# Kernel tuning notes

Measured on AMD Instinct MI355X. Metric: run time of the kernel, lower is better.

The kernel has to match this reference:

```python
import jax, jax.numpy as jnp
import numpy as np

N_NODES = 500_000
N_EDGES = 16_000_000


def gcn_conv(x, src, dst, ew, W, b, n_nodes):
    # PyG GCNConv: add self-loops (weight 1), symmetric normalization,
    # message = norm * (x @ W)[src], aggregate sum at dst, then + bias.
    loop = jnp.arange(n_nodes, dtype=src.dtype)
    src_f = jnp.concatenate([src, loop])
    dst_f = jnp.concatenate([dst, loop])
    ew_f = jnp.concatenate([ew, jnp.ones((n_nodes,), dtype=ew.dtype)])
    deg = jax.ops.segment_sum(ew_f, dst_f, num_segments=n_nodes)  # in-degree incl. self-loop
    dis = jnp.where(deg > 0, jax.lax.rsqrt(jnp.maximum(deg, 1e-12)), 0.0)
    norm = dis[src_f] * ew_f * dis[dst_f]  # [E+N]
    h = x @ W  # [N, out]
    msg = h[src_f] * norm[:, None]  # gather + scale
    out = jax.ops.segment_sum(msg, dst_f, num_segments=n_nodes)  # scatter-add
    return out + b


def setup_inputs() -> dict:
    key = jax.random.key(0)
    k = jax.random.split(key, 8)
    x = jax.random.normal(k[0], (N_NODES, 1), dtype=jnp.float32)
    edge_index = jax.random.randint(k[1], (2, N_EDGES), 0, N_NODES, dtype=jnp.int64)
    edge_weight = jax.random.uniform(k[2], (N_EDGES,), dtype=jnp.float32)
    W1 = jax.random.normal(k[3], (1, 16), dtype=jnp.float32)
    b1 = jax.random.normal(k[4], (16,), dtype=jnp.float32) * 0.1
    W2 = jax.random.normal(k[5], (16, 2), dtype=jnp.float32)
    b2 = jax.random.normal(k[6], (2,), dtype=jnp.float32) * 0.1
    return {"x": x, "edge_index": edge_index, "edge_weight": edge_weight,
            "W1": W1, "b1": b1, "W2": W2, "b2": b2}


def reference(x, edge_index, edge_weight, W1, b1, W2, b2):
    src, dst = edge_index[0], edge_index[1]
    n = x.shape[0]
    h = gcn_conv(x, src, dst, edge_weight, W1, b1, n)
    h = jax.nn.relu(h)
    # F.dropout(training=self.training): eval mode -> identity
    h = gcn_conv(h, src, dst, edge_weight, W2, b2, n)
    s = jnp.sum(h, axis=0)[None, :]  # [1, 2]
    return jax.nn.softmax(s, axis=1)
```

## Files before the change

### kernel.cpp

```cpp
#include <hip/hip_runtime.h>
#include <math.h>

constexpr int N_NODES   = 500000;
constexpr int N_EDGES   = 16000000;
constexpr int BSHIFT    = 12;
constexpr int BSZ       = 1 << BSHIFT;
constexpr int NB        = (N_NODES + BSZ - 1) / BSZ;
constexpr int CHK       = 6144;
constexpr int NCHK      = (N_EDGES + CHK - 1) / CHK;
constexpr int SPB_SHIFT = 4;
constexpr int SPB       = 1 << SPB_SHIFT;


__global__ __launch_bounds__(256) void k_count1(const int* __restrict__ dst,
                                                unsigned* __restrict__ counts) {
    __shared__ unsigned hist[NB];
    int c = blockIdx.x;
    for (int t = threadIdx.x; t < NB; t += 256) hist[t] = 0;
    __syncthreads();
    int lo = c * CHK, hi = min(lo + CHK, N_EDGES);
    for (int e = lo + threadIdx.x; e < hi; e += 256)
        atomicAdd(&hist[dst[e] >> BSHIFT], 1u);
    __syncthreads();
    for (int b = threadIdx.x; b < NB; b += 256)
        counts[(size_t)b * NCHK + c] = hist[b];
}

__global__ __launch_bounds__(256) void k_rowscan(const unsigned* __restrict__ counts,
                                                 unsigned* __restrict__ bases,
                                                 unsigned* __restrict__ rowsum) {
    __shared__ unsigned tile[256];
    __shared__ unsigned carry;
    int b = blockIdx.x;
    if (threadIdx.x == 0) carry = 0;
    __syncthreads();
    for (int t0 = 0; t0 < NCHK; t0 += 256) {
        int c = t0 + threadIdx.x;
        unsigned v = (c < NCHK) ? counts[(size_t)b * NCHK + c] : 0u;
        tile[threadIdx.x] = v;
        __syncthreads();
#pragma unroll
        for (int off = 1; off < 256; off <<= 1) {
            unsigned u = (threadIdx.x >= off) ? tile[threadIdx.x - off] : 0u;
            __syncthreads();
            tile[threadIdx.x] += u;
            __syncthreads();
        }
        unsigned excl = tile[threadIdx.x] - v;
        if (c < NCHK) bases[(size_t)b * NCHK + c] = carry + excl;
        __syncthreads();
        if (threadIdx.x == 0) carry += tile[255];
        __syncthreads();
    }
    if (threadIdx.x == 0) rowsum[b] = carry;
}

__global__ __launch_bounds__(128) void k_bucketscan(const unsigned* __restrict__ rowsum,
                                                    unsigned* __restrict__ offsets1) {
    __shared__ unsigned tile[128];
    int t = threadIdx.x;
    unsigned v = (t < NB) ? rowsum[t] : 0u;
    tile[t] = v;
    __syncthreads();
#pragma unroll
    for (int off = 1; off < 128; off <<= 1) {
        unsigned u = (t >= off) ? tile[t - off] : 0u;
        __syncthreads();
        tile[t] += u;
        __syncthreads();
    }
    if (t < NB) offsets1[t] = tile[t] - v;
    if (t == 0) offsets1[NB] = tile[127];
}

__global__ __launch_bounds__(256) void k_scatter1(const int* __restrict__ src,
                                                  const int* __restrict__ dst,
                                                  const float* __restrict__ w,
                                                  const unsigned* __restrict__ bases,
                                                  const unsigned* __restrict__ offsets1,
                                                  uint2* __restrict__ A) {
    __shared__ uint2    buf[CHK];
    __shared__ unsigned hist[NB];
    __shared__ unsigned coff[NB + 1];
    __shared__ unsigned cur[NB];
    __shared__ int      gbase[NB];
    int c = blockIdx.x;
    int lo = c * CHK, hi = min(lo + CHK, N_EDGES);
    int n = hi - lo;
    for (int t = threadIdx.x; t < NB; t += 256) { hist[t] = 0; cur[t] = 0; }
    __syncthreads();
    for (int e = lo + threadIdx.x; e < hi; e += 256)
        atomicAdd(&hist[dst[e] >> BSHIFT], 1u);
    __syncthreads();
    {
        __shared__ unsigned sc[128];
        int t = threadIdx.x;
        if (t < 128) sc[t] = (t < NB) ? hist[t] : 0u;
        __syncthreads();
#pragma unroll
        for (int off = 1; off < 128; off <<= 1) {
            unsigned u = 0;
            if (t < 128 && t >= off) u = sc[t - off];
            __syncthreads();
            if (t < 128) sc[t] += u;
            __syncthreads();
        }
        if (t < NB) coff[t] = sc[t] - hist[t];
        if (t == 0) coff[NB] = (unsigned)n;
        __syncthreads();
        if (t < NB)
            gbase[t] = (int)(offsets1[t] + bases[(size_t)t * NCHK + c]) - (int)coff[t];
    }
    __syncthreads();
    for (int e = lo + threadIdx.x; e < hi; e += 256) {
        int d = dst[e];
        int b = d >> BSHIFT;
        unsigned p = coff[b] + atomicAdd(&cur[b], 1u);
        buf[p] = make_uint2(((unsigned)(d & (BSZ - 1)) << 19) | (unsigned)src[e],
                            __float_as_uint(w[e]));
    }
    __syncthreads();
    for (int i = threadIdx.x; i < n; i += 256) {
        int blo = 0, bhi = NB;
        while (blo + 1 < bhi) {
            int m = (blo + bhi) >> 1;
            if ((int)coff[m] <= i) blo = m; else bhi = m;
        }
        A[gbase[blo] + i] = buf[i];
    }
}

__device__ __forceinline__ void slice_bounds(const unsigned* offsets1,
                                             int& b, int& e0, int& e1) {
    b = blockIdx.x >> SPB_SHIFT;
    int s = blockIdx.x & (SPB - 1);
    int base = (int)offsets1[b];
    int len  = (int)offsets1[b + 1] - base;
    e0 = base + (int)(((long long)len * s) >> SPB_SHIFT);
    e1 = base + (int)(((long long)len * (s + 1)) >> SPB_SHIFT);
}

__global__ __launch_bounds__(256) void k_deg(const uint2* __restrict__ A,
                                             const unsigned* __restrict__ offsets1,
                                             float* __restrict__ staging) {
    __shared__ float bins[BSZ];
    for (int i = threadIdx.x; i < BSZ; i += 256) bins[i] = 0.0f;
    int b, e0, e1;
    slice_bounds(offsets1, b, e0, e1);
    __syncthreads();
    for (int e = e0 + threadIdx.x; e < e1; e += 256) {
        uint2 a = A[e];
        atomicAdd(&bins[a.x >> 19], __uint_as_float(a.y));
    }
    __syncthreads();
    float* out = staging + (size_t)blockIdx.x * BSZ;
    for (int i = threadIdx.x; i < BSZ; i += 256) out[i] = bins[i];
}

__global__ __launch_bounds__(256) void k_dis(const float* __restrict__ staging,
                                             const float* __restrict__ x,
                                             float* __restrict__ dis,
                                             float* __restrict__ y) {
    int i = blockIdx.x * 256 + threadIdx.x;
    if (i >= N_NODES) return;
    int b = i >> BSHIFT, dl = i & (BSZ - 1);
    const float* st = staging + ((size_t)b << (BSHIFT + SPB_SHIFT)) + dl;
    float deg = 1.0f;
#pragma unroll
    for (int s = 0; s < SPB; ++s) deg += st[(size_t)s << BSHIFT];
    float d = rsqrtf(deg);
    dis[i] = d;
    y[i]   = d * x[i];
}

__global__ __launch_bounds__(256) void k_in(const uint2* __restrict__ A,
                                            const unsigned* __restrict__ offsets1,
                                            const float* __restrict__ y,
                                            float* __restrict__ staging) {
    __shared__ float bins[BSZ];
    for (int i = threadIdx.x; i < BSZ; i += 256) bins[i] = 0.0f;
    int b, e0, e1;
    slice_bounds(offsets1, b, e0, e1);
    __syncthreads();
    for (int e = e0 + threadIdx.x; e < e1; e += 256) {
        uint2 a = A[e];
        float yv = y[a.x & 0x7FFFFu];
        atomicAdd(&bins[a.x >> 19], __uint_as_float(a.y) * yv);
    }
    __syncthreads();
    float* out = staging + (size_t)blockIdx.x * BSZ;
    for (int i = threadIdx.x; i < BSZ; i += 256) out[i] = bins[i];
}

__global__ __launch_bounds__(256) void k_h(const float* __restrict__ staging,
                                           const float* __restrict__ dis,
                                           const float* __restrict__ x,
                                           const float* __restrict__ W1,
                                           const float* __restrict__ b1,
                                           const float* __restrict__ W2,
                                           float2* __restrict__ g2,
                                           float* __restrict__ sacc) {
    int i = blockIdx.x * 256 + threadIdx.x;
    float c0 = 0.0f, c1 = 0.0f;
    if (i < N_NODES) {
        int b = i >> BSHIFT, dl = i & (BSZ - 1);
        const float* st = staging + ((size_t)b << (BSHIFT + SPB_SHIFT)) + dl;
        float inagg = 0.0f;
#pragma unroll
        for (int s = 0; s < SPB; ++s) inagg += st[(size_t)s << BSHIFT];
        float dv   = dis[i];
        float agg1 = dv * (inagg + dv * x[i]);
        float h0 = 0.0f, h1 = 0.0f;
#pragma unroll
        for (int j = 0; j < 16; ++j) {
            float a = fmaxf(fmaf(agg1, W1[j], b1[j]), 0.0f);
            h0 = fmaf(a, W2[2 * j + 0], h0);
            h1 = fmaf(a, W2[2 * j + 1], h1);
        }
        g2[i] = make_float2(dv * h0, dv * h1);
        c0 = dv * dv * h0;
        c1 = dv * dv * h1;
    }
#pragma unroll
    for (int off = 32; off > 0; off >>= 1) {
        c0 += __shfl_down(c0, off, 64);
        c1 += __shfl_down(c1, off, 64);
    }
    __shared__ float red0[4], red1[4];
    int wave = threadIdx.x >> 6, lane = threadIdx.x & 63;
    if (lane == 0) { red0[wave] = c0; red1[wave] = c1; }
    __syncthreads();
    if (threadIdx.x == 0) {
        atomicAdd(&sacc[0], red0[0] + red0[1] + red0[2] + red0[3]);
        atomicAdd(&sacc[1], red1[0] + red1[1] + red1[2] + red1[3]);
    }
}

__global__ __launch_bounds__(256) void k_out(const uint2* __restrict__ A,
                                             const unsigned* __restrict__ offsets1,
                                             const float* __restrict__ dis,
                                             const float2* __restrict__ g2,
                                             float* __restrict__ sacc) {
    __shared__ float disL[BSZ];
    int b, e0, e1;
    slice_bounds(offsets1, b, e0, e1);
    int nbase = b << BSHIFT;
    for (int i = threadIdx.x; i < BSZ; i += 256) {
        int node = nbase + i;
        disL[i] = (node < N_NODES) ? dis[node] : 0.0f;
    }
    __syncthreads();
    float c0 = 0.0f, c1 = 0.0f;
    for (int e = e0 + threadIdx.x; e < e1; e += 256) {
        uint2 a = A[e];
        float2 g = g2[a.x & 0x7FFFFu];
        float wd = __uint_as_float(a.y) * disL[a.x >> 19];
        c0 = fmaf(wd, g.x, c0);
        c1 = fmaf(wd, g.y, c1);
    }
#pragma unroll
    for (int off = 32; off > 0; off >>= 1) {
        c0 += __shfl_down(c0, off, 64);
        c1 += __shfl_down(c1, off, 64);
    }
    __shared__ float red0[4], red1[4];
    int wave = threadIdx.x >> 6, lane = threadIdx.x & 63;
    if (lane == 0) { red0[wave] = c0; red1[wave] = c1; }
    __syncthreads();
    if (threadIdx.x == 0) {
        atomicAdd(&sacc[0], red0[0] + red0[1] + red0[2] + red0[3]);
        atomicAdd(&sacc[1], red1[0] + red1[1] + red1[2] + red1[3]);
    }
}

__global__ void k_final(const float* __restrict__ sacc,
                        const float* __restrict__ b2,
                        float* __restrict__ out) {
    if (threadIdx.x == 0 && blockIdx.x == 0) {
        float s0 = sacc[0] + (float)N_NODES * b2[0];
        float s1 = sacc[1] + (float)N_NODES * b2[1];
        float m = fmaxf(s0, s1);
        float e0 = __expf(s0 - m);
        float e1 = __expf(s1 - m);
        float inv = 1.0f / (e0 + e1);
        out[0] = e0 * inv;
        out[1] = e1 * inv;
    }
}


__global__ __launch_bounds__(256) void k_init_fb(float* __restrict__ deg,
                                                 float* __restrict__ inagg,
                                                 float* __restrict__ outco,
                                                 float* __restrict__ sacc) {
    int i = blockIdx.x * blockDim.x + threadIdx.x;
    if (i < N_NODES) { deg[i] = 1.0f; inagg[i] = 0.0f; outco[i] = 0.0f; }
    if (i < 2) sacc[i] = 0.0f;
}

__global__ __launch_bounds__(256) void k_deg_fb(const int4* __restrict__ dst4,
                                                const float4* __restrict__ w4,
                                                float* __restrict__ deg) {
    int i = blockIdx.x * blockDim.x + threadIdx.x;
    int4 d = dst4[i]; float4 w = w4[i];
    atomicAdd(&deg[d.x], w.x); atomicAdd(&deg[d.y], w.y);
    atomicAdd(&deg[d.z], w.z); atomicAdd(&deg[d.w], w.w);
}

__global__ __launch_bounds__(256) void k_dis_fb(float* __restrict__ degdis,
                                                const float* __restrict__ x,
                                                float* __restrict__ y) {
    int i = blockIdx.x * blockDim.x + threadIdx.x;
    if (i < N_NODES) { float d = rsqrtf(degdis[i]); degdis[i] = d; y[i] = d * x[i]; }
}

__global__ __launch_bounds__(256) void k_edge2_fb(const int4* __restrict__ src4,
                                                  const int4* __restrict__ dst4,
                                                  const float4* __restrict__ w4,
                                                  const float* __restrict__ dis,
                                                  const float* __restrict__ y,
                                                  float* __restrict__ inagg,
                                                  float* __restrict__ outco) {
    int i = blockIdx.x * blockDim.x + threadIdx.x;
    int4 s = src4[i]; int4 d = dst4[i]; float4 w = w4[i];
    atomicAdd(&inagg[d.x], w.x * y[s.x]); atomicAdd(&inagg[d.y], w.y * y[s.y]);
    atomicAdd(&inagg[d.z], w.z * y[s.z]); atomicAdd(&inagg[d.w], w.w * y[s.w]);
    atomicAdd(&outco[s.x], w.x * dis[d.x]); atomicAdd(&outco[s.y], w.y * dis[d.y]);
    atomicAdd(&outco[s.z], w.z * dis[d.z]); atomicAdd(&outco[s.w], w.w * dis[d.w]);
}

__global__ __launch_bounds__(256) void k_node_fb(const float* __restrict__ dis,
                                                 const float* __restrict__ x,
                                                 const float* __restrict__ inagg,
                                                 const float* __restrict__ outco,
                                                 const float* __restrict__ W1,
                                                 const float* __restrict__ b1,
                                                 const float* __restrict__ W2,
                                                 float* __restrict__ sacc) {
    int i = blockIdx.x * blockDim.x + threadIdx.x;
    float c0 = 0.0f, c1 = 0.0f;
    if (i < N_NODES) {
        float dv = dis[i];
        float agg1 = dv * (inagg[i] + dv * x[i]);
        float coef = dv * outco[i] + dv * dv;
        float h0 = 0.0f, h1 = 0.0f;
#pragma unroll
        for (int j = 0; j < 16; ++j) {
            float a = fmaxf(fmaf(agg1, W1[j], b1[j]), 0.0f);
            h0 = fmaf(a, W2[2 * j + 0], h0);
            h1 = fmaf(a, W2[2 * j + 1], h1);
        }
        c0 = coef * h0; c1 = coef * h1;
    }
#pragma unroll
    for (int off = 32; off > 0; off >>= 1) {
        c0 += __shfl_down(c0, off, 64);
        c1 += __shfl_down(c1, off, 64);
    }
    __shared__ float red0[4], red1[4];
    int wave = threadIdx.x >> 6, lane = threadIdx.x & 63;
    if (lane == 0) { red0[wave] = c0; red1[wave] = c1; }
    __syncthreads();
    if (threadIdx.x == 0) {
        atomicAdd(&sacc[0], red0[0] + red0[1] + red0[2] + red0[3]);
        atomicAdd(&sacc[1], red1[0] + red1[1] + red1[2] + red1[3]);
    }
}

extern "C" void kernel_launch(void* const* d_in, const int* in_sizes, int n_in,
                              void* d_out, int out_size, void* d_ws, size_t ws_size,
                              hipStream_t stream) {
    const float* x  = (const float*)d_in[0];
    int*         ei = (int*)d_in[1];
    const float* ew = (const float*)d_in[2];
    const float* W1 = (const float*)d_in[3];
    const float* b1 = (const float*)d_in[4];
    const float* W2 = (const float*)d_in[5];
    const float* b2 = (const float*)d_in[6];
    float* out = (float*)d_out;

    const int* src = ei;
    const int* dst = ei + N_EDGES;

    const int TB = 256;
    const int nodeBlocks = (N_NODES + TB - 1) / TB;

    char* base = (char*)d_ws;
    uint2*    A   = (uint2*)base;
    float*    y   = (float*)(base + 128000000);
    float*    dis = (float*)(base + 130000000);
    float2*   g2  = (float2*)(base + 132000000);
    unsigned* counts   = (unsigned*)(base + 136000000);
    unsigned* bases    = counts + (size_t)NB * NCHK;
    unsigned* offsets1 = bases + (size_t)NB * NCHK;
    unsigned* rowsum   = offsets1 + (NB + 1);
    float*    sacc     = (float*)(rowsum + NB);
    const size_t fastNeed = (size_t)((char*)(sacc + 2) - base) + 64;

    if (ws_size >= fastNeed) {
        float* staging = (float*)ei;

        hipMemsetAsync(sacc, 0, 2 * sizeof(float), stream);

        k_count1<<<NCHK, TB, 0, stream>>>(dst, counts);
        k_rowscan<<<NB, TB, 0, stream>>>(counts, bases, rowsum);
        k_bucketscan<<<1, 128, 0, stream>>>(rowsum, offsets1);
        k_scatter1<<<NCHK, TB, 0, stream>>>(src, dst, ew, bases, offsets1, A);
        k_deg<<<NB * SPB, TB, 0, stream>>>(A, offsets1, staging);
        k_dis<<<nodeBlocks, TB, 0, stream>>>(staging, x, dis, y);
        k_in<<<NB * SPB, TB, 0, stream>>>(A, offsets1, y, staging);
        k_h<<<nodeBlocks, TB, 0, stream>>>(staging, dis, x, W1, b1, W2, g2, sacc);
        k_out<<<NB * SPB, TB, 0, stream>>>(A, offsets1, dis, g2, sacc);
        k_final<<<1, 64, 0, stream>>>(sacc, b2, out);
    } else {
        float* ws     = (float*)d_ws;
        float* degdis = ws;
        float* yf     = ws + N_NODES;
        float* inaggf = ws + 2 * N_NODES;
        float* outcof = ws + 3 * N_NODES;
        float* saccf  = ws + 4 * N_NODES;
        const int edgeBlocks = (N_EDGES / 4) / TB;

        k_init_fb<<<nodeBlocks, TB, 0, stream>>>(degdis, inaggf, outcof, saccf);
        k_deg_fb<<<edgeBlocks, TB, 0, stream>>>((const int4*)dst, (const float4*)ew, degdis);
        k_dis_fb<<<nodeBlocks, TB, 0, stream>>>(degdis, x, yf);
        k_edge2_fb<<<edgeBlocks, TB, 0, stream>>>((const int4*)src, (const int4*)dst,
                                                  (const float4*)ew, degdis, yf, inaggf, outcof);
        k_node_fb<<<nodeBlocks, TB, 0, stream>>>(degdis, x, inaggf, outcof, W1, b1, W2, saccf);
        k_final<<<1, 64, 0, stream>>>(saccf, b2, out);
    }
}
```

Before: 795.2 us.

## Vectorize edge loads, shrink chunk size, and write buckets per-wave in scatter

Edge loads in the count and scatter kernels now use int4/float4 vectors, four edges per thread per iteration. The chunk size drops from 6144 to 4096, which gives more blocks, less shared memory per block and a larger counts matrix. The write-out loop no longer does a binary search per element; each wave now copies whole bucket runs contiguously. The aim is less instruction overhead and better-coalesced global writes, at the cost of more per-chunk scan work and relying on the edge count being divisible by 4.

```diff
diff --git a/kernel.cpp b/kernel.cpp
--- a/kernel.cpp
+++ b/kernel.cpp
@@ -6,21 +6,27 @@
 constexpr int BSHIFT    = 12;
 constexpr int BSZ       = 1 << BSHIFT;
 constexpr int NB        = (N_NODES + BSZ - 1) / BSZ;
-constexpr int CHK       = 6144;
+constexpr int CHK       = 4096;
 constexpr int NCHK      = (N_EDGES + CHK - 1) / CHK;
 constexpr int SPB_SHIFT = 4;
 constexpr int SPB       = 1 << SPB_SHIFT;
 
 
-__global__ __launch_bounds__(256) void k_count1(const int* __restrict__ dst,
+__global__ __launch_bounds__(256) void k_count1(const int4* __restrict__ dst4,
                                                 unsigned* __restrict__ counts) {
     __shared__ unsigned hist[NB];
     int c = blockIdx.x;
     for (int t = threadIdx.x; t < NB; t += 256) hist[t] = 0;
     __syncthreads();
-    int lo = c * CHK, hi = min(lo + CHK, N_EDGES);
-    for (int e = lo + threadIdx.x; e < hi; e += 256)
-        atomicAdd(&hist[dst[e] >> BSHIFT], 1u);
+    int lo4 = c * (CHK / 4);
+    int hi4 = min(lo4 + CHK / 4, N_EDGES / 4);
+    for (int q = lo4 + threadIdx.x; q < hi4; q += 256) {
+        int4 d = dst4[q];
+        atomicAdd(&hist[d.x >> BSHIFT], 1u);
+        atomicAdd(&hist[d.y >> BSHIFT], 1u);
+        atomicAdd(&hist[d.z >> BSHIFT], 1u);
+        atomicAdd(&hist[d.w >> BSHIFT], 1u);
+    }
     __syncthreads();
     for (int b = threadIdx.x; b < NB; b += 256)
         counts[(size_t)b * NCHK + c] = hist[b];
@@ -73,9 +79,9 @@
     if (t == 0) offsets1[NB] = tile[127];
 }
 
-__global__ __launch_bounds__(256) void k_scatter1(const int* __restrict__ src,
-                                                  const int* __restrict__ dst,
-                                                  const float* __restrict__ w,
+__global__ __launch_bounds__(256) void k_scatter1(const int4* __restrict__ src4,
+                                                  const int4* __restrict__ dst4,
+                                                  const float4* __restrict__ w4,
                                                   const unsigned* __restrict__ bases,
                                                   const unsigned* __restrict__ offsets1,
                                                   uint2* __restrict__ A) {
@@ -84,16 +90,22 @@
     __shared__ unsigned coff[NB + 1];
     __shared__ unsigned cur[NB];
     __shared__ int      gbase[NB];
+    __shared__ unsigned sc[128];
     int c = blockIdx.x;
-    int lo = c * CHK, hi = min(lo + CHK, N_EDGES);
-    int n = hi - lo;
+    int lo4 = c * (CHK / 4);
+    int hi4 = min(lo4 + CHK / 4, N_EDGES / 4);
+    int n = (hi4 - lo4) * 4;
     for (int t = threadIdx.x; t < NB; t += 256) { hist[t] = 0; cur[t] = 0; }
     __syncthreads();
-    for (int e = lo + threadIdx.x; e < hi; e += 256)
-        atomicAdd(&hist[dst[e] >> BSHIFT], 1u);
+    for (int q = lo4 + threadIdx.x; q < hi4; q += 256) {
+        int4 d = dst4[q];
+        atomicAdd(&hist[d.x >> BSHIFT], 1u);
+        atomicAdd(&hist[d.y >> BSHIFT], 1u);
+        atomicAdd(&hist[d.z >> BSHIFT], 1u);
+        atomicAdd(&hist[d.w >> BSHIFT], 1u);
+    }
     __syncthreads();
     {
-        __shared__ unsigned sc[128];
         int t = threadIdx.x;
         if (t < 128) sc[t] = (t < NB) ? hist[t] : 0u;
         __syncthreads();
@@ -112,21 +124,43 @@
             gbase[t] = (int)(offsets1[t] + bases[(size_t)t * NCHK + c]) - (int)coff[t];
     }
     __syncthreads();
-    for (int e = lo + threadIdx.x; e < hi; e += 256) {
-        int d = dst[e];
-        int b = d >> BSHIFT;
-        unsigned p = coff[b] + atomicAdd(&cur[b], 1u);
-        buf[p] = make_uint2(((unsigned)(d & (BSZ - 1)) << 19) | (unsigned)src[e],
-                            __float_as_uint(w[e]));
-    }
-    __syncthreads();
-    for (int i = threadIdx.x; i < n; i += 256) {
-        int blo = 0, bhi = NB;
-        while (blo + 1 < bhi) {
-            int m = (blo + bhi) >> 1;
-            if ((int)coff[m] <= i) blo = m; else bhi = m;
-        }
-        A[gbase[blo] + i] = buf[i];
+    for (int q = lo4 + threadIdx.x; q < hi4; q += 256) {
+        int4   s = src4[q];
+        int4   d = dst4[q];
+        float4 w = w4[q];
+        {
+            int b = d.x >> BSHIFT;
+            unsigned p = coff[b] + atomicAdd(&cur[b], 1u);
+            buf[p] = make_uint2(((unsigned)(d.x & (BSZ - 1)) << 19) | (unsigned)s.x,
+                                __float_as_uint(w.x));
+        }
+        {
+            int b = d.y >> BSHIFT;
+            unsigned p = coff[b] + atomicAdd(&cur[b], 1u);
+            buf[p] = make_uint2(((unsigned)(d.y & (BSZ - 1)) << 19) | (unsigned)s.y,
+                                __float_as_uint(w.y));
+        }
+        {
+            int b = d.z >> BSHIFT;
+            unsigned p = coff[b] + atomicAdd(&cur[b], 1u);
+            buf[p] = make_uint2(((unsigned)(d.z & (BSZ - 1)) << 19) | (unsigned)s.z,
+                                __float_as_uint(w.z));
+        }
+        {
+            int b = d.w >> BSHIFT;
+            unsigned p = coff[b] + atomicAdd(&cur[b], 1u);
+            buf[p] = make_uint2(((unsigned)(d.w & (BSZ - 1)) << 19) | (unsigned)s.w,
+                                __float_as_uint(w.w));
+        }
+    }
+    __syncthreads();
+    int wave = threadIdx.x >> 6;
+    int lane = threadIdx.x & 63;
+    for (int b = wave; b < NB; b += 4) {
+        int r0 = (int)coff[b], r1 = (int)coff[b + 1];
+        int gb = gbase[b];
+        for (int i = r0 + lane; i < r1; i += 64)
+            A[gb + i] = buf[i];
     }
 }
 
@@ -402,10 +436,11 @@
 
         hipMemsetAsync(sacc, 0, 2 * sizeof(float), stream);
 
-        k_count1<<<NCHK, TB, 0, stream>>>(dst, counts);
+        k_count1<<<NCHK, TB, 0, stream>>>((const int4*)dst, counts);
         k_rowscan<<<NB, TB, 0, stream>>>(counts, bases, rowsum);
         k_bucketscan<<<1, 128, 0, stream>>>(rowsum, offsets1);
-        k_scatter1<<<NCHK, TB, 0, stream>>>(src, dst, ew, bases, offsets1, A);
+        k_scatter1<<<NCHK, TB, 0, stream>>>((const int4*)src, (const int4*)dst,
+                                            (const float4*)ew, bases, offsets1, A);
         k_deg<<<NB * SPB, TB, 0, stream>>>(A, offsets1, staging);
         k_dis<<<nodeBlocks, TB, 0, stream>>>(staging, x, dis, y);
         k_in<<<NB * SPB, TB, 0, stream>>>(A, offsets1, y, staging);
```

Result: faster. 676.7 us (-14.9%).
